# Optimization experiments

Measured on AMD Instinct MI355X. Metric: run time of the kernel, lower is better.

Reference implementation:

```python
import math
import jax, jax.numpy as jnp
import numpy as np

B, L, D, H = 2, 2048, 1024, 16
HD = D // H  # 64

def setup_inputs() -> dict:
    key = jax.random.key(0)
    k1, k2, k3 = jax.random.split(key, 3)
    x = jax.random.normal(k1, (B, L, D), dtype=jnp.float32)
    Wqkv = jax.random.normal(k2, (3 * D, D), dtype=jnp.float32) * (1.0 / math.sqrt(D))
    Wo = jax.random.normal(k3, (D, D), dtype=jnp.float32) * (1.0 / math.sqrt(D))
    return {"x": x, "Wqkv": Wqkv, "Wo": Wo}

def reference(x, Wqkv, Wo):
    # QKV projection (torch Linear: y = x @ W.T), then split
    qkv = jnp.einsum('bld,ed->ble', x, Wqkv)  # [B, L, 3D]
    q, k, v = jnp.split(qkv, 3, axis=-1)
    # [B, H, L, HD]
    q = q.reshape(B, L, H, HD).transpose(0, 2, 1, 3)
    k = k.reshape(B, L, H, HD).transpose(0, 2, 1, 3)
    v = v.reshape(B, L, H, HD).transpose(0, 2, 1, 3)
    # scores; causal mask applied before the 1/sqrt(d) scale (as in source;
    # -inf is unchanged by scaling so math matches scale-then-mask)
    scores = jnp.einsum('bhqd,bhkd->bhqk', q, k)
    causal = jnp.tril(jnp.ones((L, L), dtype=bool))
    scores = jnp.where(causal, scores, -jnp.inf)
    attn = jax.nn.softmax(scores / math.sqrt(HD), axis=-1)
    out = jnp.einsum('bhqk,bhkd->bhqd', attn, v)  # [B, H, L, HD]
    out = out.transpose(0, 2, 1, 3).reshape(B, L, D)
    # output projection (dropout is identity in eval / p=0)
    return jnp.einsum('bld,ed->ble', out, Wo)
```

## Files before the change

kernel.cpp:

```cpp
#include <hip/hip_runtime.h>
#include <hip/hip_bf16.h>
#include <cstdint>
#include <cstddef>

#define B_SZ 2
#define L_SEQ 2048
#define DM 1024
#define NH 16
#define HDIM 64
#define BL (B_SZ * L_SEQ)
#define QKV_N (3 * DM)

typedef __attribute__((ext_vector_type(4))) float f32x4;
typedef __attribute__((ext_vector_type(16))) float f32x16;
typedef __attribute__((ext_vector_type(8))) short bf16x8;
typedef __attribute__((ext_vector_type(4))) unsigned int u32x4;
typedef unsigned short u16;
typedef __attribute__((ext_vector_type(4))) unsigned short u16x4;

__device__ __forceinline__ float bf2f(u16 u) {
  union { unsigned int i; float f; } c; c.i = ((unsigned int)u) << 16; return c.f;
}
__device__ __forceinline__ u16 f2bf(float f) {
  union { float f; unsigned int i; } c; c.f = f;
  unsigned int r = c.i + 0x7fffu + ((c.i >> 16) & 1u);
  return (u16)(r >> 16);
}

__device__ __forceinline__ void gload_lds16(const void* g, void* l) {
  __builtin_amdgcn_global_load_lds(
      (const __attribute__((address_space(1))) void*)g,
      (__attribute__((address_space(3))) void*)l, 16, 0, 0);
}

__device__ __forceinline__ f32x16 mfma32(bf16x8 a, bf16x8 b, f32x16 c) {
  return __builtin_amdgcn_mfma_f32_32x32x16_bf16(a, b, c, 0, 0, 0);
}

__device__ __forceinline__ unsigned cvtpk(float lo, float hi) {
  unsigned r;
  asm("v_cvt_pk_bf16_f32 %0, %1, %2" : "=v"(r) : "v"(lo), "v"(hi));
  return r;
}
__device__ __forceinline__ void plswap(unsigned& a, unsigned& b) {
  asm("v_permlane32_swap_b32 %0, %1" : "+v"(a), "+v"(b));
}

template <int BASE>
__device__ __forceinline__ bf16x8 pack_bfrag(const f32x16& v) {
  unsigned a  = cvtpk(v[BASE + 0], v[BASE + 1]);
  unsigned a2 = cvtpk(v[BASE + 2], v[BASE + 3]);
  unsigned b  = cvtpk(v[BASE + 4], v[BASE + 5]);
  unsigned b2 = cvtpk(v[BASE + 6], v[BASE + 7]);
  plswap(a, b);
  plswap(a2, b2);
  u32x4 fw; fw[0] = a; fw[1] = a2; fw[2] = b; fw[3] = b2;
  return __builtin_bit_cast(bf16x8, fw);
}

__global__ __launch_bounds__(256) void cvt_f32_bf16(const float* __restrict__ in,
                                                    u16* __restrict__ out, int n4) {
  int i = blockIdx.x * blockDim.x + threadIdx.x;
  const int stride = gridDim.x * blockDim.x;
  for (; i < n4; i += stride) {
    float4 v = ((const float4*)in)[i];
    u16x4 o;
    o[0] = f2bf(v.x); o[1] = f2bf(v.y); o[2] = f2bf(v.z); o[3] = f2bf(v.w);
    ((u16x4*)out)[i] = o;
  }
}

template <bool BF16_OUT>
__global__ __launch_bounds__(256) void gemm_bt(
    const u16* __restrict__ A, const u16* __restrict__ B,
    void* __restrict__ Cv, int M, int N, int K) {
  __shared__ u16 As[128 * 32];
  __shared__ u16 Bs[128 * 32];
  const int tid = threadIdx.x;
  const int lane = tid & 63, w = tid >> 6;
  const int lr = lane & 15, lg = lane >> 4;
  const int wr = w >> 1, wc = w & 1;
  const int bm = blockIdx.y * 128, bn = blockIdx.x * 128;

  f32x4 acc[4][4] = {};

  const int l4 = lane >> 2;
  const int csw = ((lane & 3) ^ ((lane >> 3) & 3)) * 8;
  const size_t aoff0 = (size_t)(bm + (w * 2 + 0) * 16 + l4) * K + csw;
  const size_t aoff1 = (size_t)(bm + (w * 2 + 1) * 16 + l4) * K + csw;
  const size_t boff0 = (size_t)(bn + (w * 2 + 0) * 16 + l4) * K + csw;
  const size_t boff1 = (size_t)(bn + (w * 2 + 1) * 16 + l4) * K + csw;
  u16* As0 = As + (w * 2 + 0) * 512;
  u16* As1 = As + (w * 2 + 1) * 512;
  u16* Bs0 = Bs + (w * 2 + 0) * 512;
  u16* Bs1 = Bs + (w * 2 + 1) * 512;
  const int sw_rd = (lr >> 1) & 3;

  for (int k0 = 0; k0 < K; k0 += 32) {
    gload_lds16(A + aoff0 + k0, As0);
    gload_lds16(A + aoff1 + k0, As1);
    gload_lds16(B + boff0 + k0, Bs0);
    gload_lds16(B + boff1 + k0, Bs1);
    __syncthreads();

    bf16x8 af[4], bfr[4];
#pragma unroll
    for (int mt = 0; mt < 4; ++mt) {
      const int row = wr * 64 + mt * 16 + lr;
      af[mt] = *(const bf16x8*)&As[row * 32 + ((lg ^ sw_rd) * 8)];
    }
#pragma unroll
    for (int nt = 0; nt < 4; ++nt) {
      const int row = wc * 64 + nt * 16 + lr;
      bfr[nt] = *(const bf16x8*)&Bs[row * 32 + ((lg ^ sw_rd) * 8)];
    }
#pragma unroll
    for (int mt = 0; mt < 4; ++mt)
#pragma unroll
      for (int nt = 0; nt < 4; ++nt)
        acc[mt][nt] = __builtin_amdgcn_mfma_f32_16x16x32_bf16(af[mt], bfr[nt],
                                                              acc[mt][nt], 0, 0, 0);
    __syncthreads();
  }

#pragma unroll
  for (int mt = 0; mt < 4; ++mt)
#pragma unroll
    for (int nt = 0; nt < 4; ++nt)
#pragma unroll
      for (int r = 0; r < 4; ++r) {
        const int row = bm + wr * 64 + mt * 16 + lg * 4 + r;
        const int col = bn + wc * 64 + nt * 16 + lr;
        if (BF16_OUT)
          ((u16*)Cv)[(size_t)row * N + col] = f2bf(acc[mt][nt][r]);
        else
          ((float*)Cv)[(size_t)row * N + col] = acc[mt][nt][r];
      }
}

__device__ const uint8_t JQT[40] = {15,15,15,15, 14,14,14, 13,13,13, 12,12,12,
                                    11,11,11, 10,10, 9,9, 8,8, 7,7, 6, 5, 4, 3,
                                    14, 10, 6, 2, 13, 9, 5, 1, 12, 8, 4, 0};
__device__ const uint8_t JT0[40] = {0,8,16,24, 0,8,16, 0,8,16, 0,8,16,
                                    0,8,16, 0,8, 0,8, 0,8, 0,8, 0, 0, 0, 0,
                                    24, 16, 8, 0, 24, 16, 8, 0, 24, 16, 8, 0};
__device__ const uint8_t JT1[40] = {8,16,24,32, 8,16,24, 8,16,24, 8,16,24,
                                    8,16,24, 8,16, 8,16, 8,16, 8,16, 8, 8, 8, 8,
                                    30, 22, 14, 6, 28, 20, 12, 4, 26, 18, 10, 2};
__device__ const uint8_t SBASE[16] = {255,255,255,255, 0,2,4,6,
                                      8,11,14,17, 20,24,28,32};

__global__ __launch_bounds__(256) void attn_fused(const u16* __restrict__ qkv,
                                                  u16* __restrict__ aout,
                                                  u16* __restrict__ opart_lo,
                                                  u16* __restrict__ opart_hi,
                                                  float2* __restrict__ mlb) {
  __shared__ u16 Kl[2][64 * 64];
  __shared__ u16 Vt[2][64 * 64];

  const int tid = threadIdx.x;
  const int lane = tid & 63, w = tid >> 6;
  const int l31 = lane & 31, hi = lane >> 5;
  const int id = (int)blockIdx.x;
  const int bh = id & 31, j = id >> 5;
  const int qt = JQT[j];
  const int t0 = JT0[j], t1 = JT1[j];
  const int b = bh >> 4, h = bh & 15;
  const u16* base = qkv + (size_t)b * L_SEQ * QKV_N;
  const int W = qt * 128 + w * 32;
  const int qrow = W + l31;

  const int krow = tid >> 2;
  const int ks0 = (tid & 3) * 2;
  const int kr7 = krow & 7;
  const u16* gpk_base = base + (size_t)krow * QKV_N + DM + h * HDIM + ks0 * 8;
  bf16x8 kr0, kr1;

  const int vd0 = (tid & 31) * 2;
  const int vkb = tid >> 5;
  const int vge = tid & 7;
  const int vgo = (tid & 7) ^ 4;
  const u16* gpv_base = base + (size_t)(vkb * 8) * QKV_N + 2 * DM + h * HDIM + vd0;
  unsigned int vtmp[8];

  auto issue_loads = [&](int t) {
    const u16* gpk = gpk_base + (size_t)t * 64 * QKV_N;
    kr0 = *(const bf16x8*)(gpk);
    kr1 = *(const bf16x8*)(gpk + 8);
    const u16* gpv = gpv_base + (size_t)t * 64 * QKV_N;
#pragma unroll
    for (int jj = 0; jj < 8; ++jj)
      vtmp[jj] = *(const unsigned int*)(gpv + (size_t)jj * QKV_N);
  };
  auto write_lds = [&](int buf) {
    *(bf16x8*)&Kl[buf][krow * 64 + ((ks0 ^ kr7) * 8)] = kr0;
    *(bf16x8*)&Kl[buf][krow * 64 + (((ks0 + 1) ^ kr7) * 8)] = kr1;
    u32x4 lo, hiw;
#pragma unroll
    for (int jj = 0; jj < 4; ++jj) {
      lo[jj]  = __builtin_amdgcn_perm(vtmp[2 * jj + 1], vtmp[2 * jj], 0x05040100u);
      hiw[jj] = __builtin_amdgcn_perm(vtmp[2 * jj + 1], vtmp[2 * jj], 0x07060302u);
    }
    *(u32x4*)&Vt[buf][vd0 * 64 + ((vkb ^ vge) * 8)] = lo;
    *(u32x4*)&Vt[buf][(vd0 + 1) * 64 + ((vkb ^ vgo) * 8)] = hiw;
  };

  bf16x8 bq[4];
  {
    const u16* qp = base + (size_t)qrow * QKV_N + h * HDIM + hi * 8;
#pragma unroll
    for (int dc = 0; dc < 4; ++dc) {
      bf16x8 tq = *(const bf16x8*)(qp + dc * 16);
#pragma unroll
      for (int i = 0; i < 8; ++i)
        tq[i] = (short)f2bf(bf2f((u16)tq[i]) * 0.18033688f);
      bq[dc] = tq;
    }
  }

  f32x16 acc0 = {}, acc1 = {};
  float mrow = -1e30f, lrow = 0.f;

  const int vg = ((l31 >> 1) & 7) ^ ((l31 & 1) << 2);
  const int lsw = l31 & 7;

  issue_loads(t0);
  write_lds(0);
  __syncthreads();

  for (int t = t0; t < t1; ++t) {
    const int cur = (t - t0) & 1;
    if (t + 1 < t1) issue_loads(t + 1);

    if (64 * t <= W + 31) {
      f32x16 s0 = {}, s1 = {};
#pragma unroll
      for (int dc = 0; dc < 4; ++dc) {
        const int sl = ((dc * 2 + hi) ^ lsw) * 8;
        const bf16x8 k0 = *(const bf16x8*)&Kl[cur][l31 * 64 + sl];
        const bf16x8 k1 = *(const bf16x8*)&Kl[cur][(32 + l31) * 64 + sl];
        s0 = mfma32(k0, bq[dc], s0);
        s1 = mfma32(k1, bq[dc], s1);
      }

      if (64 * t + 63 > W) {
#pragma unroll
        for (int r = 0; r < 16; ++r) {
          const int kg = t * 64 + (r & 3) + 8 * (r >> 2) + 4 * hi;
          if (kg > qrow) s0[r] = -1e30f;
          if (kg + 32 > qrow) s1[r] = -1e30f;
        }
      }

      float mx[8];
#pragma unroll
      for (int i = 0; i < 8; ++i)
        mx[i] = fmaxf(fmaxf(s0[i], s0[i + 8]), fmaxf(s1[i], s1[i + 8]));
#pragma unroll
      for (int i = 0; i < 4; ++i) mx[i] = fmaxf(mx[i], mx[i + 4]);
      float px = fmaxf(fmaxf(mx[0], mx[2]), fmaxf(mx[1], mx[3]));
      px = fmaxf(px, __shfl_xor(px, 32));

      if (!__all(px <= mrow + 8.f)) {
        const float mnew = fmaxf(mrow, px);
        const float alpha = exp2f(mrow - mnew);
        mrow = mnew;
        lrow *= alpha;
#pragma unroll
        for (int i = 0; i < 16; ++i) { acc0[i] *= alpha; acc1[i] *= alpha; }
      }

#pragma unroll
      for (int r = 0; r < 16; ++r) {
        s0[r] = exp2f(s0[r] - mrow);
        s1[r] = exp2f(s1[r] - mrow);
      }
      float sm[8];
#pragma unroll
      for (int i = 0; i < 8; ++i)
        sm[i] = (s0[i] + s0[i + 8]) + (s1[i] + s1[i + 8]);
#pragma unroll
      for (int i = 0; i < 4; ++i) sm[i] += sm[i + 4];
      float rs = (sm[0] + sm[2]) + (sm[1] + sm[3]);
      rs += __shfl_xor(rs, 32);
      lrow += rs;

      const bf16x8 pf0 = pack_bfrag<0>(s0);
      const bf16x8 pf1 = pack_bfrag<8>(s0);
      const bf16x8 pf2 = pack_bfrag<0>(s1);
      const bf16x8 pf3 = pack_bfrag<8>(s1);

#pragma unroll
      for (int c = 0; c < 4; ++c) {
        const bf16x8 pf = c == 0 ? pf0 : c == 1 ? pf1 : c == 2 ? pf2 : pf3;
        const int sl = ((c * 2 + hi) ^ vg) * 8;
        const bf16x8 va = *(const bf16x8*)&Vt[cur][l31 * 64 + sl];
        const bf16x8 vb = *(const bf16x8*)&Vt[cur][(32 + l31) * 64 + sl];
        acc0 = mfma32(va, pf, acc0);
        acc1 = mfma32(vb, pf, acc1);
      }
    }

    if (t + 1 < t1) write_lds(((t + 1) - t0) & 1);
    __syncthreads();
  }

  if (SBASE[qt] != 255) {
    const int c = t0 >> 3;
    const int slot = ((int)SBASE[qt] + c) * 32 + bh;
    u16* po = slot < 1024 ? opart_lo + (size_t)slot * 8192
                          : opart_hi + (size_t)(slot - 1024) * 8192;
    const int q = w * 32 + l31;
#pragma unroll
    for (int i = 0; i < 16; ++i) {
      const int d0 = (i & 3) + 8 * (i >> 2) + 4 * hi;
      po[d0 * 128 + q] = f2bf(acc0[i]);
      po[(d0 + 32) * 128 + q] = f2bf(acc1[i]);
    }
    if (hi == 0) mlb[slot * 128 + q] = make_float2(mrow, lrow);
  } else {
    const float inv = 1.f / lrow;
#pragma unroll
    for (int i = 0; i < 16; ++i) { acc0[i] *= inv; acc1[i] *= inv; }
    const bf16x8 of0 = pack_bfrag<0>(acc0);
    const bf16x8 of1 = pack_bfrag<8>(acc0);
    const bf16x8 of2 = pack_bfrag<0>(acc1);
    const bf16x8 of3 = pack_bfrag<8>(acc1);
    u16* op = aout + (size_t)(b * L_SEQ + qrow) * DM + h * HDIM + hi * 8;
    *(bf16x8*)(op + 0)  = of0;
    *(bf16x8*)(op + 16) = of1;
    *(bf16x8*)(op + 32) = of2;
    *(bf16x8*)(op + 48) = of3;
  }
}

__global__ __launch_bounds__(256) void attn_combine(
    const u16* __restrict__ opart_lo, const u16* __restrict__ opart_hi,
    const float2* __restrict__ mlb, u16* __restrict__ aout) {
  const int gid = (int)blockIdx.x * 256 + (int)threadIdx.x;
  const int q = gid & 127;
  const int u = gid >> 7;
  const int qt = 4 + (u >> 5), bh = u & 31;
  const int b = bh >> 4, h = bh & 15;
  const int nc = (2 * qt + 9) >> 3;
  const int sb = (int)SBASE[qt];

  float2 ml[4];
  const u16* pp[4];
  float mm = -1e30f;
#pragma unroll
  for (int c = 0; c < 4; ++c)
    if (c < nc) {
      const int slot = (sb + c) * 32 + bh;
      ml[c] = mlb[slot * 128 + q];
      pp[c] = slot < 1024 ? opart_lo + (size_t)slot * 8192
                          : opart_hi + (size_t)(slot - 1024) * 8192;
      mm = fmaxf(mm, ml[c].x);
    }
  float L = 0.f, cf[4];
#pragma unroll
  for (int c = 0; c < 4; ++c)
    if (c < nc) { cf[c] = exp2f(ml[c].x - mm); L += ml[c].y * cf[c]; }
  const float invl = 1.f / L;
#pragma unroll
  for (int c = 0; c < 4; ++c)
    if (c < nc) cf[c] *= invl;

  const int qrow = qt * 128 + q;
  u16* op = aout + (size_t)(b * L_SEQ + qrow) * DM + h * HDIM;
#pragma unroll
  for (int d0 = 0; d0 < 64; d0 += 8) {
    float v[8] = {};
#pragma unroll
    for (int c = 0; c < 4; ++c)
      if (c < nc) {
#pragma unroll
        for (int jj = 0; jj < 8; ++jj)
          v[jj] += cf[c] * bf2f(pp[c][(d0 + jj) * 128 + q]);
      }
    u16x4 oa, ob;
#pragma unroll
    for (int jj = 0; jj < 4; ++jj) { oa[jj] = f2bf(v[jj]); ob[jj] = f2bf(v[jj + 4]); }
    *(u16x4*)(op + d0) = oa;
    *(u16x4*)(op + d0 + 4) = ob;
  }
}

extern "C" void kernel_launch(void* const* d_in, const int* in_sizes, int n_in,
                              void* d_out, int out_size, void* d_ws, size_t ws_size,
                              hipStream_t stream) {
  (void)in_sizes; (void)n_in; (void)out_size; (void)ws_size;
  const float* x = (const float*)d_in[0];
  const float* wqkv = (const float*)d_in[1];
  const float* wo = (const float*)d_in[2];

  char* ws = (char*)d_ws;
  u16* x_bf = (u16*)(ws);
  u16* w_bf = (u16*)(ws + (size_t)(8u << 20));
  u16* wo_bf = (u16*)(ws + (size_t)(14u << 20));
  u16* qkv_bf = (u16*)(ws + (size_t)(16u << 20));
  u16* ao_bf = x_bf;
  u16* opart_lo = (u16*)d_out;
  u16* opart_hi = (u16*)(ws + (size_t)(8u << 20));
  float2* mlb = (float2*)(ws + (size_t)(10u << 20));

  cvt_f32_bf16<<<2048, 256, 0, stream>>>(x, x_bf, BL * DM / 4);
  cvt_f32_bf16<<<2048, 256, 0, stream>>>(wqkv, w_bf, QKV_N * DM / 4);
  cvt_f32_bf16<<<1024, 256, 0, stream>>>(wo, wo_bf, DM * DM / 4);

  dim3 g1(QKV_N / 128, BL / 128);
  gemm_bt<true><<<g1, 256, 0, stream>>>(x_bf, w_bf, (void*)qkv_bf, BL, QKV_N, DM);

  attn_fused<<<dim3(1280), 256, 0, stream>>>(qkv_bf, ao_bf, opart_lo, opart_hi, mlb);
  attn_combine<<<dim3(192), 256, 0, stream>>>(opart_lo, opart_hi, mlb, ao_bf);

  dim3 g3(DM / 128, BL / 128);
  gemm_bt<false><<<g3, 256, 0, stream>>>(ao_bf, wo_bf, d_out, BL, DM, DM);
}
```

Baseline: 143.6 us.

## Use 256-row query tiles with 512-thread attention blocks and fuse conversion kernels

Attention blocks now cover 256 query rows with 8 waves instead of 128 rows with 4 waves. Each K/V tile loaded into LDS is therefore reused by twice as many queries, and the grid shrinks to 640 blocks. The split-KV schedule tables, partial-output layout and combine indexing are rebuilt for the larger tiles. The three fp32-to-bf16 conversion launches are merged into one kernel to save launch overhead. The trade-offs are fewer blocks to balance the causal workload, more causal-masked waste per tile, and higher per-block resource use.

Measured after the change: 139.5 us. -2.9%, faster.

```diff
diff --git a/kernel.cpp b/kernel.cpp
--- a/kernel.cpp
+++ b/kernel.cpp
@@ -14,6 +14,7 @@
 typedef __attribute__((ext_vector_type(4))) float f32x4;
 typedef __attribute__((ext_vector_type(16))) float f32x16;
 typedef __attribute__((ext_vector_type(8))) short bf16x8;
+typedef __attribute__((ext_vector_type(2))) unsigned int u32x2;
 typedef __attribute__((ext_vector_type(4))) unsigned int u32x4;
 typedef unsigned short u16;
 typedef __attribute__((ext_vector_type(4))) unsigned short u16x4;
@@ -58,15 +59,31 @@
   return __builtin_bit_cast(bf16x8, fw);
 }
 
-__global__ __launch_bounds__(256) void cvt_f32_bf16(const float* __restrict__ in,
-                                                    u16* __restrict__ out, int n4) {
+#define N4_X  (BL * DM / 4)
+#define N4_WQ (QKV_N * DM / 4)
+#define N4_WO (DM * DM / 4)
+__global__ __launch_bounds__(256) void cvt_all(
+    const float* __restrict__ x, const float* __restrict__ wqkv,
+    const float* __restrict__ wo, u16* __restrict__ x_bf,
+    u16* __restrict__ w_bf, u16* __restrict__ wo_bf) {
   int i = blockIdx.x * blockDim.x + threadIdx.x;
   const int stride = gridDim.x * blockDim.x;
-  for (; i < n4; i += stride) {
-    float4 v = ((const float4*)in)[i];
+  const int total = N4_X + N4_WQ + N4_WO;
+  for (; i < total; i += stride) {
+    const float4* src;
+    u16x4* dst;
+    if (i < N4_X) {
+      src = (const float4*)x + i; dst = (u16x4*)x_bf + i;
+    } else if (i < N4_X + N4_WQ) {
+      src = (const float4*)wqkv + (i - N4_X); dst = (u16x4*)w_bf + (i - N4_X);
+    } else {
+      src = (const float4*)wo + (i - N4_X - N4_WQ);
+      dst = (u16x4*)wo_bf + (i - N4_X - N4_WQ);
+    }
+    float4 v = *src;
     u16x4 o;
     o[0] = f2bf(v.x); o[1] = f2bf(v.y); o[2] = f2bf(v.z); o[3] = f2bf(v.w);
-    ((u16x4*)out)[i] = o;
+    *dst = o;
   }
 }
 
@@ -138,19 +155,16 @@
       }
 }
 
-__device__ const uint8_t JQT[40] = {15,15,15,15, 14,14,14, 13,13,13, 12,12,12,
-                                    11,11,11, 10,10, 9,9, 8,8, 7,7, 6, 5, 4, 3,
-                                    14, 10, 6, 2, 13, 9, 5, 1, 12, 8, 4, 0};
-__device__ const uint8_t JT0[40] = {0,8,16,24, 0,8,16, 0,8,16, 0,8,16,
-                                    0,8,16, 0,8, 0,8, 0,8, 0,8, 0, 0, 0, 0,
-                                    24, 16, 8, 0, 24, 16, 8, 0, 24, 16, 8, 0};
-__device__ const uint8_t JT1[40] = {8,16,24,32, 8,16,24, 8,16,24, 8,16,24,
-                                    8,16,24, 8,16, 8,16, 8,16, 8,16, 8, 8, 8, 8,
-                                    30, 22, 14, 6, 28, 20, 12, 4, 26, 18, 10, 2};
-__device__ const uint8_t SBASE[16] = {255,255,255,255, 0,2,4,6,
-                                      8,11,14,17, 20,24,28,32};
-
-__global__ __launch_bounds__(256) void attn_fused(const u16* __restrict__ qkv,
+__device__ const uint8_t JST[20] = {7,7,7,7, 6,6,6, 5,5,5, 4,4, 3,3, 2, 1,
+                                    6, 4, 2, 0};
+__device__ const uint8_t JT0[20] = {0,8,16,24, 0,8,16, 0,8,16, 0,8, 0,8, 0, 0,
+                                    24, 16, 8, 0};
+__device__ const uint8_t JT1[20] = {8,16,24,32, 8,16,24, 8,16,24, 8,16, 8,16, 8, 8,
+                                    28, 20, 12, 4};
+__device__ const uint8_t SB[8]   = {255, 255, 0, 2, 4, 7, 10, 14};
+__device__ const uint8_t SCNT[8] = {1, 1, 2, 2, 3, 3, 4, 4};
+
+__global__ __launch_bounds__(512) void attn_fused(const u16* __restrict__ qkv,
                                                   u16* __restrict__ aout,
                                                   u16* __restrict__ opart_lo,
                                                   u16* __restrict__ opart_hi,
@@ -163,46 +177,42 @@
   const int l31 = lane & 31, hi = lane >> 5;
   const int id = (int)blockIdx.x;
   const int bh = id & 31, j = id >> 5;
-  const int qt = JQT[j];
+  const int st = JST[j];
   const int t0 = JT0[j], t1 = JT1[j];
   const int b = bh >> 4, h = bh & 15;
   const u16* base = qkv + (size_t)b * L_SEQ * QKV_N;
-  const int W = qt * 128 + w * 32;
+  const int W = st * 256 + w * 32;
   const int qrow = W + l31;
 
-  const int krow = tid >> 2;
-  const int ks0 = (tid & 3) * 2;
+  const int krow = tid >> 3;
+  const int ks = tid & 7;
   const int kr7 = krow & 7;
-  const u16* gpk_base = base + (size_t)krow * QKV_N + DM + h * HDIM + ks0 * 8;
-  bf16x8 kr0, kr1;
+  const u16* gpk_base = base + (size_t)krow * QKV_N + DM + h * HDIM + ks * 8;
+  bf16x8 kr;
 
   const int vd0 = (tid & 31) * 2;
-  const int vkb = tid >> 5;
+  const int vkg = tid >> 5;
   const int vge = tid & 7;
   const int vgo = (tid & 7) ^ 4;
-  const u16* gpv_base = base + (size_t)(vkb * 8) * QKV_N + 2 * DM + h * HDIM + vd0;
-  unsigned int vtmp[8];
+  const u16* gpv_base = base + (size_t)(vkg * 4) * QKV_N + 2 * DM + h * HDIM + vd0;
+  unsigned int vtmp[4];
 
   auto issue_loads = [&](int t) {
-    const u16* gpk = gpk_base + (size_t)t * 64 * QKV_N;
-    kr0 = *(const bf16x8*)(gpk);
-    kr1 = *(const bf16x8*)(gpk + 8);
+    kr = *(const bf16x8*)(gpk_base + (size_t)t * 64 * QKV_N);
     const u16* gpv = gpv_base + (size_t)t * 64 * QKV_N;
 #pragma unroll
-    for (int jj = 0; jj < 8; ++jj)
+    for (int jj = 0; jj < 4; ++jj)
       vtmp[jj] = *(const unsigned int*)(gpv + (size_t)jj * QKV_N);
   };
   auto write_lds = [&](int buf) {
-    *(bf16x8*)&Kl[buf][krow * 64 + ((ks0 ^ kr7) * 8)] = kr0;
-    *(bf16x8*)&Kl[buf][krow * 64 + (((ks0 + 1) ^ kr7) * 8)] = kr1;
-    u32x4 lo, hiw;
-#pragma unroll
-    for (int jj = 0; jj < 4; ++jj) {
-      lo[jj]  = __builtin_amdgcn_perm(vtmp[2 * jj + 1], vtmp[2 * jj], 0x05040100u);
-      hiw[jj] = __builtin_amdgcn_perm(vtmp[2 * jj + 1], vtmp[2 * jj], 0x07060302u);
-    }
-    *(u32x4*)&Vt[buf][vd0 * 64 + ((vkb ^ vge) * 8)] = lo;
-    *(u32x4*)&Vt[buf][(vd0 + 1) * 64 + ((vkb ^ vgo) * 8)] = hiw;
+    *(bf16x8*)&Kl[buf][krow * 64 + ((ks ^ kr7) * 8)] = kr;
+    u32x2 lo, hiw;
+    lo[0]  = __builtin_amdgcn_perm(vtmp[1], vtmp[0], 0x05040100u);
+    lo[1]  = __builtin_amdgcn_perm(vtmp[3], vtmp[2], 0x05040100u);
+    hiw[0] = __builtin_amdgcn_perm(vtmp[1], vtmp[0], 0x07060302u);
+    hiw[1] = __builtin_amdgcn_perm(vtmp[3], vtmp[2], 0x07060302u);
+    *(u32x2*)&Vt[buf][vd0 * 64 + (((vkg >> 1) ^ vge) * 8) + (vkg & 1) * 4] = lo;
+    *(u32x2*)&Vt[buf][(vd0 + 1) * 64 + (((vkg >> 1) ^ vgo) * 8) + (vkg & 1) * 4] = hiw;
   };
 
   bf16x8 bq[4];
@@ -305,19 +315,19 @@
     __syncthreads();
   }
 
-  if (SBASE[qt] != 255) {
+  if (SB[st] != 255) {
     const int c = t0 >> 3;
-    const int slot = ((int)SBASE[qt] + c) * 32 + bh;
-    u16* po = slot < 1024 ? opart_lo + (size_t)slot * 8192
-                          : opart_hi + (size_t)(slot - 1024) * 8192;
+    const int slot = ((int)SB[st] + c) * 32 + bh;
+    u16* po = slot < 512 ? opart_lo + (size_t)slot * 16384
+                         : opart_hi + (size_t)(slot - 512) * 16384;
     const int q = w * 32 + l31;
 #pragma unroll
     for (int i = 0; i < 16; ++i) {
       const int d0 = (i & 3) + 8 * (i >> 2) + 4 * hi;
-      po[d0 * 128 + q] = f2bf(acc0[i]);
-      po[(d0 + 32) * 128 + q] = f2bf(acc1[i]);
-    }
-    if (hi == 0) mlb[slot * 128 + q] = make_float2(mrow, lrow);
+      po[d0 * 256 + q] = f2bf(acc0[i]);
+      po[(d0 + 32) * 256 + q] = f2bf(acc1[i]);
+    }
+    if (hi == 0) mlb[slot * 256 + q] = make_float2(mrow, lrow);
   } else {
     const float inv = 1.f / lrow;
 #pragma unroll
@@ -338,12 +348,12 @@
     const u16* __restrict__ opart_lo, const u16* __restrict__ opart_hi,
     const float2* __restrict__ mlb, u16* __restrict__ aout) {
   const int gid = (int)blockIdx.x * 256 + (int)threadIdx.x;
-  const int q = gid & 127;
-  const int u = gid >> 7;
-  const int qt = 4 + (u >> 5), bh = u & 31;
+  const int q = gid & 255;
+  const int u = gid >> 8;
+  const int st = 2 + (u >> 5), bh = u & 31;
   const int b = bh >> 4, h = bh & 15;
-  const int nc = (2 * qt + 9) >> 3;
-  const int sb = (int)SBASE[qt];
+  const int nc = (int)SCNT[st];
+  const int sb = (int)SB[st];
 
   float2 ml[4];
   const u16* pp[4];
@@ -352,9 +362,9 @@
   for (int c = 0; c < 4; ++c)
     if (c < nc) {
       const int slot = (sb + c) * 32 + bh;
-      ml[c] = mlb[slot * 128 + q];
-      pp[c] = slot < 1024 ? opart_lo + (size_t)slot * 8192
-                          : opart_hi + (size_t)(slot - 1024) * 8192;
+      ml[c] = mlb[slot * 256 + q];
+      pp[c] = slot < 512 ? opart_lo + (size_t)slot * 16384
+                         : opart_hi + (size_t)(slot - 512) * 16384;
       mm = fmaxf(mm, ml[c].x);
     }
   float L = 0.f, cf[4];
@@ -366,7 +376,7 @@
   for (int c = 0; c < 4; ++c)
     if (c < nc) cf[c] *= invl;
 
-  const int qrow = qt * 128 + q;
+  const int qrow = st * 256 + q;
   u16* op = aout + (size_t)(b * L_SEQ + qrow) * DM + h * HDIM;
 #pragma unroll
   for (int d0 = 0; d0 < 64; d0 += 8) {
@@ -376,7 +386,7 @@
       if (c < nc) {
 #pragma unroll
         for (int jj = 0; jj < 8; ++jj)
-          v[jj] += cf[c] * bf2f(pp[c][(d0 + jj) * 128 + q]);
+          v[jj] += cf[c] * bf2f(pp[c][(d0 + jj) * 256 + q]);
       }
     u16x4 oa, ob;
 #pragma unroll
@@ -404,14 +414,12 @@
   u16* opart_hi = (u16*)(ws + (size_t)(8u << 20));
   float2* mlb = (float2*)(ws + (size_t)(10u << 20));
 
-  cvt_f32_bf16<<<2048, 256, 0, stream>>>(x, x_bf, BL * DM / 4);
-  cvt_f32_bf16<<<2048, 256, 0, stream>>>(wqkv, w_bf, QKV_N * DM / 4);
-  cvt_f32_bf16<<<1024, 256, 0, stream>>>(wo, wo_bf, DM * DM / 4);
+  cvt_all<<<2048, 256, 0, stream>>>(x, wqkv, wo, x_bf, w_bf, wo_bf);
 
   dim3 g1(QKV_N / 128, BL / 128);
   gemm_bt<true><<<g1, 256, 0, stream>>>(x_bf, w_bf, (void*)qkv_bf, BL, QKV_N, DM);
 
-  attn_fused<<<dim3(1280), 256, 0, stream>>>(qkv_bf, ao_bf, opart_lo, opart_hi, mlb);
+  attn_fused<<<dim3(640), 512, 0, stream>>>(qkv_bf, ao_bf, opart_lo, opart_hi, mlb);
   attn_combine<<<dim3(192), 256, 0, stream>>>(opart_lo, opart_hi, mlb, ao_bf);
 
   dim3 g3(DM / 128, BL / 128);
```
